# Optimization experiments

Measured on AMD Instinct MI355X. Metric: run time of the kernel, lower is better.

## Reference

```python
import jax, jax.numpy as jnp
import numpy as np

N_NODES = 100000
N_EDGES = 3200000


def gcn_conv(x, W, b, src, dst, n_nodes):
    """PyG GCNConv: self-loops, symmetric D^-1/2 A D^-1/2 norm, linear, bias."""
    loop = jnp.arange(n_nodes, dtype=src.dtype)
    s = jnp.concatenate([src, loop])  # [E+N]
    d = jnp.concatenate([dst, loop])  # [E+N]
    # degree computed at destination (col), edge_weight = 1
    deg = jax.ops.segment_sum(jnp.ones_like(d, dtype=x.dtype), d,
                              num_segments=n_nodes)
    dinv = jnp.where(deg > 0, jax.lax.rsqrt(deg), 0.0)
    norm = dinv[s] * dinv[d]  # [E+N]
    h = x @ W.T  # [N, out]
    msg = h[s] * norm[:, None]  # gather + scale, [E+N, out]
    out = jax.ops.segment_sum(msg, d, num_segments=n_nodes)  # scatter-add
    return out + b


def setup_inputs() -> dict:
    key = jax.random.key(0)
    k1, k2, k3, k4 = jax.random.split(key, 4)
    x = jax.random.normal(k1, (N_NODES, 2), dtype=jnp.float32)
    edge_index = jax.random.randint(k2, (2, N_EDGES), 0, N_NODES,
                                    dtype=jnp.int64)
    # Glorot-ish init for linear weights
    W1 = jax.random.normal(k3, (64, 2), dtype=jnp.float32) * 0.5
    b1 = jnp.zeros((64,), dtype=jnp.float32)
    W2 = jax.random.normal(k4, (2, 64), dtype=jnp.float32) * 0.125
    b2 = jnp.zeros((2,), dtype=jnp.float32)
    return {"x": x, "edge_index": edge_index, "W1": W1, "b1": b1,
            "W2": W2, "b2": b2}


def reference(x, edge_index, W1, b1, W2, b2):
    src, dst = edge_index[0], edge_index[1]
    h = gcn_conv(x, W1, b1, src, dst, N_NODES)
    h = jax.nn.relu(h)
    out = gcn_conv(h, W2, b2, src, dst, N_NODES)
    return out
```

## Files before the change

### kernel.cpp

```cpp
#include <hip/hip_runtime.h>

#define N_NODES 100000
#define SHIFT 7
#define BNODES 128
#define NB 782
#define CAP 5120
#define CAPR 768
#define TILE 8192
#define SB 1024


__global__ __launch_bounds__(SB, 8) void k_sort(const int* __restrict__ src,
                                                const int* __restrict__ dst,
                                                int* claim,
                                                const int* __restrict__ pz,
                                                int* sg, int e) {
    __shared__ int hist[2 * NB];
    __shared__ int rank[2 * NB];
    __shared__ int addrbase[NB];
    __shared__ int partials[16];
    __shared__ int stage[TILE];
    __shared__ unsigned short binmap[TILE];

    const int t = threadIdx.x;
    const int base = blockIdx.x * TILE;
    const int reg7 = blockIdx.x & 7;
    const int n = min(TILE, e - base);
    const int goff = (t >> 9) * NB;

    for (int i = t; i < 2 * NB; i += SB) hist[i] = 0;
    __syncthreads();

    int recs[8];
    int bins[8];
    int* myh = hist + goff;
#pragma unroll
    for (int k = 0; k < 2; ++k) {
        int idx = base + (k * SB + t) * 4;
        if (idx + 3 < e) {
            int4 s4 = *(const int4*)(src + idx);
            int4 d4 = *(const int4*)(dst + idx);
            int ss[4] = {s4.x, s4.y, s4.z, s4.w};
            int dd[4] = {d4.x, d4.y, d4.z, d4.w};
#pragma unroll
            for (int j = 0; j < 4; ++j) {
                int b = dd[j] >> SHIFT;
                bins[4 * k + j] = b;
                recs[4 * k + j] = ss[j] | ((dd[j] & (BNODES - 1)) << 17);
                atomicAdd(&myh[b], 1);
            }
        } else {
#pragma unroll
            for (int j = 0; j < 4; ++j) {
                int i2 = idx + j;
                if (i2 < e) {
                    int d = dst[i2];
                    int b = d >> SHIFT;
                    bins[4 * k + j] = b;
                    recs[4 * k + j] = src[i2] | ((d & (BNODES - 1)) << 17);
                    atomicAdd(&myh[b], 1);
                } else {
                    bins[4 * k + j] = -1;
                }
            }
        }
    }
    __syncthreads();

    int c0 = 0, c1 = 0, c = 0;
    if (t < NB) {
        c0 = hist[t];
        c1 = hist[NB + t];
        c = c0 + c1;
    }
    int vs = c;
#pragma unroll
    for (int off = 1; off < 64; off <<= 1) {
        int w = __shfl_up(vs, off, 64);
        if ((t & 63) >= off) vs += w;
    }
    if ((t & 63) == 63) partials[t >> 6] = vs;
    __syncthreads();
    int add = 0;
    for (int w = 0; w < (t >> 6); ++w) add += partials[w];
    vs += add;
    int excl = vs - c;
    const int P = *pz;
    if (t < NB) {
        rank[t] = excl;
        rank[NB + t] = excl + c0;
        int rb = c ? (atomicAdd(&claim[reg7 * NB + t], c) - P) : 0;
        addrbase[t] = (reg7 * NB + t) * CAPR + rb - excl;
    }
    __syncthreads();

    int* myr = rank + goff;
#pragma unroll
    for (int m = 0; m < 8; ++m) {
        int b = bins[m];
        if (b >= 0) {
            int pos = atomicAdd(&myr[b], 1);
            stage[pos] = recs[m];
            binmap[pos] = (unsigned short)b;
        }
    }
    __syncthreads();

    for (int i = t; i < n; i += SB) {
        sg[addrbase[binmap[i]] + i] = stage[i];
    }
}

__global__ __launch_bounds__(512) void k_refine(const int* __restrict__ claim,
                                                const int* __restrict__ pz,
                                                const int* __restrict__ sg,
                                                const float* __restrict__ x,
                                                int* sg2, int* packed,
                                                float2* u) {
    __shared__ int hist[4 * BNODES];
    __shared__ int rank[4 * BNODES];
    __shared__ int partials[2];
    const int t = threadIdx.x;
    const int b = blockIdx.x;
    const int P = *pz;
    const int g = t >> 7;

    for (int i = t; i < 4 * BNODES; i += 512) hist[i] = 0;
    __syncthreads();

    int* myh = hist + g * BNODES;
#pragma unroll
    for (int r = 0; r < 8; ++r) {
        const int len = claim[r * NB + b] - P;
        const int* pr = sg + (r * NB + b) * CAPR;
        for (int i = t; i < len; i += 512) {
            atomicAdd(&myh[((unsigned)pr[i]) >> 17], 1);
        }
    }
    __syncthreads();

    int c4x = 0, c4y = 0, c4z = 0, c4w = 0, tot = 0;
    if (t < BNODES) {
        c4x = hist[t];
        c4y = hist[BNODES + t];
        c4z = hist[2 * BNODES + t];
        c4w = hist[3 * BNODES + t];
        tot = (c4x + c4y) + (c4z + c4w);
    }
    int vs = tot;
#pragma unroll
    for (int off = 1; off < 64; off <<= 1) {
        int w = __shfl_up(vs, off, 64);
        if ((t & 63) >= off) vs += w;
    }
    if ((t & 63) == 63 && t < BNODES) partials[t >> 6] = vs;
    __syncthreads();
    if (t < BNODES) {
        int add = 0;
        for (int w = 0; w < (t >> 6); ++w) add += partials[w];
        vs += add;
        int excl = vs - tot;
        int run = excl;
        rank[t] = run; run += c4x;
        rank[BNODES + t] = run; run += c4y;
        rank[2 * BNODES + t] = run; run += c4z;
        rank[3 * BNODES + t] = run;
        int node = b * BNODES + t;
        if (node < N_NODES) {
            packed[node] = (b * CAP + excl) | (tot << 22);
            float dv = rsqrtf((float)(tot + 1));
            float2 xv = ((const float2*)x)[node];
            u[node] = make_float2(dv * xv.x, dv * xv.y);
        }
    }
    __syncthreads();

    int* q = sg2 + b * CAP;
    int* myr = rank + g * BNODES;
#pragma unroll
    for (int r = 0; r < 8; ++r) {
        const int len = claim[r * NB + b] - P;
        const int* pr = sg + (r * NB + b) * CAPR;
        for (int i = t; i < len; i += 512) {
            int rec = pr[i];
            q[atomicAdd(&myr[((unsigned)rec) >> 17], 1)] = rec & 0x1FFFF;
        }
    }
}

__global__ __launch_bounds__(256) void k_agg1(const int* __restrict__ sg2,
                                              const int* __restrict__ packed,
                                              const float2* __restrict__ u,
                                              const float* __restrict__ W1,
                                              const float* __restrict__ b1,
                                              const float* __restrict__ W2,
                                              float2* v) {
    __shared__ float sW1[128], sb1[64], sW2[128];
    int t = threadIdx.x;
    if (t < 128) { sW1[t] = W1[t]; sW2[t] = W2[t]; }
    else if (t < 192) sb1[t - 128] = b1[t - 128];
    __syncthreads();
    int n = blockIdx.x * 32 + (t >> 3);
    if (n >= N_NODES) return;
    int g = t & 7;
    int pk = packed[n];
    int s = pk & 0x3FFFFF;
    int cnt = ((unsigned)pk) >> 22;
    int e2 = s + cnt;
    float sx = 0.f, sy = 0.f;
    int i = s + g;
    for (; i + 24 < e2; i += 32) {
        float2 ga = u[sg2[i]];
        float2 gb = u[sg2[i + 8]];
        float2 gc = u[sg2[i + 16]];
        float2 gd = u[sg2[i + 24]];
        sx += (ga.x + gb.x) + (gc.x + gd.x);
        sy += (ga.y + gb.y) + (gc.y + gd.y);
    }
    for (; i + 8 < e2; i += 16) {
        float2 ga = u[sg2[i]];
        float2 gb = u[sg2[i + 8]];
        sx += ga.x + gb.x;
        sy += ga.y + gb.y;
    }
    if (i < e2) { float2 ga = u[sg2[i]]; sx += ga.x; sy += ga.y; }
    sx += __shfl_xor(sx, 1, 8); sy += __shfl_xor(sy, 1, 8);
    sx += __shfl_xor(sx, 2, 8); sy += __shfl_xor(sy, 2, 8);
    sx += __shfl_xor(sx, 4, 8); sy += __shfl_xor(sy, 4, 8);
    float dv = rsqrtf((float)(cnt + 1));
    float2 un = u[n];
    float a0 = dv * (sx + un.x), a1 = dv * (sy + un.y);
    float y0 = 0.f, y1 = 0.f;
#pragma unroll
    for (int k = 0; k < 8; ++k) {
        int j = g + 8 * k;
        float h = fmaxf(fmaf(sW1[2 * j], a0,
                        fmaf(sW1[2 * j + 1], a1, sb1[j])), 0.f);
        y0 = fmaf(sW2[j], h, y0);
        y1 = fmaf(sW2[64 + j], h, y1);
    }
    y0 += __shfl_xor(y0, 1, 8); y1 += __shfl_xor(y1, 1, 8);
    y0 += __shfl_xor(y0, 2, 8); y1 += __shfl_xor(y1, 2, 8);
    y0 += __shfl_xor(y0, 4, 8); y1 += __shfl_xor(y1, 4, 8);
    if (g == 0) v[n] = make_float2(dv * y0, dv * y1);
}

__global__ __launch_bounds__(256) void k_agg2(const int* __restrict__ sg2,
                                              const int* __restrict__ packed,
                                              const float2* __restrict__ v,
                                              const float* __restrict__ b2,
                                              float2* out) {
    int t = threadIdx.x;
    int n = blockIdx.x * 32 + (t >> 3);
    if (n >= N_NODES) return;
    int g = t & 7;
    int pk = packed[n];
    int s = pk & 0x3FFFFF;
    int cnt = ((unsigned)pk) >> 22;
    int e2 = s + cnt;
    float sx = 0.f, sy = 0.f;
    int i = s + g;
    for (; i + 24 < e2; i += 32) {
        float2 ga = v[sg2[i]];
        float2 gb = v[sg2[i + 8]];
        float2 gc = v[sg2[i + 16]];
        float2 gd = v[sg2[i + 24]];
        sx += (ga.x + gb.x) + (gc.x + gd.x);
        sy += (ga.y + gb.y) + (gc.y + gd.y);
    }
    for (; i + 8 < e2; i += 16) {
        float2 ga = v[sg2[i]];
        float2 gb = v[sg2[i + 8]];
        sx += ga.x + gb.x;
        sy += ga.y + gb.y;
    }
    if (i < e2) { float2 ga = v[sg2[i]]; sx += ga.x; sy += ga.y; }
    sx += __shfl_xor(sx, 1, 8); sy += __shfl_xor(sy, 1, 8);
    sx += __shfl_xor(sx, 2, 8); sy += __shfl_xor(sy, 2, 8);
    sx += __shfl_xor(sx, 4, 8); sy += __shfl_xor(sy, 4, 8);
    if (g == 0) {
        float dv = rsqrtf((float)(cnt + 1));
        float2 vn = v[n];
        out[n] = make_float2(fmaf(dv, sx + vn.x, b2[0]),
                             fmaf(dv, sy + vn.y, b2[1]));
    }
}

extern "C" void kernel_launch(void* const* d_in, const int* in_sizes, int n_in,
                              void* d_out, int out_size, void* d_ws, size_t ws_size,
                              hipStream_t stream) {
    const float* x  = (const float*)d_in[0];
    const int* ei   = (const int*)d_in[1];
    const float* W1 = (const float*)d_in[2];
    const float* b1 = (const float*)d_in[3];
    const float* W2 = (const float*)d_in[4];
    const float* b2 = (const float*)d_in[5];

    int e = in_sizes[1] / 2;
    const int* src = ei;
    const int* dst = ei + e;

    int* ws      = (int*)d_ws;
    int* claim   = ws;
    int* pz      = ws + 8 * NB;
    int* sg      = ws + 6260;
    int* sg2     = sg + 8 * NB * CAPR;
    int* packed  = sg2 + NB * CAP;
    float2* u    = (float2*)(packed + N_NODES);
    float2* v    = u + N_NODES;
    float2* outp = (float2*)d_out;

    const int gA = (N_NODES + 31) / 32;
    k_sort  <<<(e + TILE - 1) / TILE, SB, 0, stream>>>(src, dst, claim, pz, sg, e);
    k_refine<<<NB, 512, 0, stream>>>(claim, pz, sg, x, sg2, packed, u);
    k_agg1  <<<gA, 256, 0, stream>>>(sg2, packed, u, W1, b1, W2, v);
    k_agg2  <<<gA, 256, 0, stream>>>(sg2, packed, v, b2, outp);
}
```

Measured before the change: 144.9 us.

## Pad per-node edge lists to multiples of four and load indices as int4

The per-node CSR segments are now padded so each node's edge list starts 16-byte aligned. This lets the aggregation kernels read four source indices at once with int4 loads and issue four gathers per iteration under predicated masks. Separately, the first sort kernel's shared-memory histogram is split into four sub-histograms instead of two, to cut atomic contention. The costs are extra shared memory, some padding slots in the index buffer, and the assumption that CAP still holds the padded totals.

```diff
diff --git a/kernel.cpp b/kernel.cpp
--- a/kernel.cpp
+++ b/kernel.cpp
@@ -15,8 +15,8 @@
                                                 int* claim,
                                                 const int* __restrict__ pz,
                                                 int* sg, int e) {
-    __shared__ int hist[2 * NB];
-    __shared__ int rank[2 * NB];
+    __shared__ int hist[4 * NB];
+    __shared__ int rank[4 * NB];
     __shared__ int addrbase[NB];
     __shared__ int partials[16];
     __shared__ int stage[TILE];
@@ -26,9 +26,9 @@
     const int base = blockIdx.x * TILE;
     const int reg7 = blockIdx.x & 7;
     const int n = min(TILE, e - base);
-    const int goff = (t >> 9) * NB;
-
-    for (int i = t; i < 2 * NB; i += SB) hist[i] = 0;
+    const int goff = (t >> 8) * NB;
+
+    for (int i = t; i < 4 * NB; i += SB) hist[i] = 0;
     __syncthreads();
 
     int recs[8];
@@ -67,11 +67,13 @@
     }
     __syncthreads();
 
-    int c0 = 0, c1 = 0, c = 0;
+    int c0 = 0, c1 = 0, c2 = 0, c3 = 0, c = 0;
     if (t < NB) {
         c0 = hist[t];
         c1 = hist[NB + t];
-        c = c0 + c1;
+        c2 = hist[2 * NB + t];
+        c3 = hist[3 * NB + t];
+        c = (c0 + c1) + (c2 + c3);
     }
     int vs = c;
 #pragma unroll
@@ -87,8 +89,11 @@
     int excl = vs - c;
     const int P = *pz;
     if (t < NB) {
-        rank[t] = excl;
-        rank[NB + t] = excl + c0;
+        int run = excl;
+        rank[t] = run; run += c0;
+        rank[NB + t] = run; run += c1;
+        rank[2 * NB + t] = run; run += c2;
+        rank[3 * NB + t] = run;
         int rb = c ? (atomicAdd(&claim[reg7 * NB + t], c) - P) : 0;
         addrbase[t] = (reg7 * NB + t) * CAPR + rb - excl;
     }
@@ -139,15 +144,16 @@
     }
     __syncthreads();
 
-    int c4x = 0, c4y = 0, c4z = 0, c4w = 0, tot = 0;
+    int c4x = 0, c4y = 0, c4z = 0, c4w = 0, tot = 0, tot4 = 0;
     if (t < BNODES) {
         c4x = hist[t];
         c4y = hist[BNODES + t];
         c4z = hist[2 * BNODES + t];
         c4w = hist[3 * BNODES + t];
         tot = (c4x + c4y) + (c4z + c4w);
-    }
-    int vs = tot;
+        tot4 = (tot + 3) & ~3;
+    }
+    int vs = tot4;
 #pragma unroll
     for (int off = 1; off < 64; off <<= 1) {
         int w = __shfl_up(vs, off, 64);
@@ -159,7 +165,7 @@
         int add = 0;
         for (int w = 0; w < (t >> 6); ++w) add += partials[w];
         vs += add;
-        int excl = vs - tot;
+        int excl = vs - tot4;
         int run = excl;
         rank[t] = run; run += c4x;
         rank[BNODES + t] = run; run += c4y;
@@ -206,24 +212,20 @@
     int pk = packed[n];
     int s = pk & 0x3FFFFF;
     int cnt = ((unsigned)pk) >> 22;
-    int e2 = s + cnt;
     float sx = 0.f, sy = 0.f;
-    int i = s + g;
-    for (; i + 24 < e2; i += 32) {
-        float2 ga = u[sg2[i]];
-        float2 gb = u[sg2[i + 8]];
-        float2 gc = u[sg2[i + 16]];
-        float2 gd = u[sg2[i + 24]];
-        sx += (ga.x + gb.x) + (gc.x + gd.x);
-        sy += (ga.y + gb.y) + (gc.y + gd.y);
-    }
-    for (; i + 8 < e2; i += 16) {
-        float2 ga = u[sg2[i]];
-        float2 gb = u[sg2[i + 8]];
-        sx += ga.x + gb.x;
-        sy += ga.y + gb.y;
-    }
-    if (i < e2) { float2 ga = u[sg2[i]]; sx += ga.x; sy += ga.y; }
+    for (int i = 4 * g; i < cnt; i += 32) {
+        int4 q = *(const int4*)(sg2 + s + i);
+        bool p1 = i + 1 < cnt, p2 = i + 2 < cnt, p3 = i + 3 < cnt;
+        int i0 = q.x;
+        int i1 = p1 ? q.y : 0;
+        int i2 = p2 ? q.z : 0;
+        int i3 = p3 ? q.w : 0;
+        float2 g0 = u[i0], g1 = u[i1], g2 = u[i2], g3 = u[i3];
+        sx += g0.x; sy += g0.y;
+        if (p1) { sx += g1.x; sy += g1.y; }
+        if (p2) { sx += g2.x; sy += g2.y; }
+        if (p3) { sx += g3.x; sy += g3.y; }
+    }
     sx += __shfl_xor(sx, 1, 8); sy += __shfl_xor(sy, 1, 8);
     sx += __shfl_xor(sx, 2, 8); sy += __shfl_xor(sy, 2, 8);
     sx += __shfl_xor(sx, 4, 8); sy += __shfl_xor(sy, 4, 8);
@@ -257,24 +259,20 @@
     int pk = packed[n];
     int s = pk & 0x3FFFFF;
     int cnt = ((unsigned)pk) >> 22;
-    int e2 = s + cnt;
     float sx = 0.f, sy = 0.f;
-    int i = s + g;
-    for (; i + 24 < e2; i += 32) {
-        float2 ga = v[sg2[i]];
-        float2 gb = v[sg2[i + 8]];
-        float2 gc = v[sg2[i + 16]];
-        float2 gd = v[sg2[i + 24]];
-        sx += (ga.x + gb.x) + (gc.x + gd.x);
-        sy += (ga.y + gb.y) + (gc.y + gd.y);
-    }
-    for (; i + 8 < e2; i += 16) {
-        float2 ga = v[sg2[i]];
-        float2 gb = v[sg2[i + 8]];
-        sx += ga.x + gb.x;
-        sy += ga.y + gb.y;
-    }
-    if (i < e2) { float2 ga = v[sg2[i]]; sx += ga.x; sy += ga.y; }
+    for (int i = 4 * g; i < cnt; i += 32) {
+        int4 q = *(const int4*)(sg2 + s + i);
+        bool p1 = i + 1 < cnt, p2 = i + 2 < cnt, p3 = i + 3 < cnt;
+        int i0 = q.x;
+        int i1 = p1 ? q.y : 0;
+        int i2 = p2 ? q.z : 0;
+        int i3 = p3 ? q.w : 0;
+        float2 g0 = v[i0], g1 = v[i1], g2 = v[i2], g3 = v[i3];
+        sx += g0.x; sy += g0.y;
+        if (p1) { sx += g1.x; sy += g1.y; }
+        if (p2) { sx += g2.x; sy += g2.y; }
+        if (p3) { sx += g3.x; sy += g3.y; }
+    }
     sx += __shfl_xor(sx, 1, 8); sy += __shfl_xor(sy, 1, 8);
     sx += __shfl_xor(sx, 2, 8); sy += __shfl_xor(sy, 2, 8);
     sx += __shfl_xor(sx, 4, 8); sy += __shfl_xor(sy, 4, 8);
```

Result: no change. 147.5 us (+1.8%).
